# Optimization experiments

Hardware: AMD Instinct MI355X
Metric: run time of the kernel (lower is better)

Reference implementation:

```python
import jax, jax.numpy as jnp
import numpy as np

N = 100000
E = 1600000
IN_C = 512
OUT_C = 128


def setup_inputs() -> dict:
    key = jax.random.key(0)
    k1, k2, k3, k4 = jax.random.split(key, 4)
    x = jax.random.normal(k1, (N, IN_C), dtype=jnp.float32)
    edge_index = jax.random.randint(k2, (2, E), 0, N, dtype=jnp.int64)
    # GCNConv parameters (glorot weight, zero bias as in PyG defaults)
    scale = jnp.sqrt(6.0 / (IN_C + OUT_C)).astype(jnp.float32)
    W = jax.random.uniform(k3, (IN_C, OUT_C), dtype=jnp.float32, minval=-scale, maxval=scale)
    b = jnp.zeros((OUT_C,), dtype=jnp.float32)
    return {"x": x, "edge_index": edge_index, "W": W, "b": b}


def reference(x, edge_index, W, b):
    n = x.shape[0]
    loops = jnp.arange(n, dtype=edge_index.dtype)
    src = jnp.concatenate([edge_index[0], loops])  # [E+N] message sources
    dst = jnp.concatenate([edge_index[1], loops])  # [E+N] message targets
    # symmetric GCN normalization: deg over targets incl. self-loops
    deg = jax.ops.segment_sum(jnp.ones_like(src, dtype=x.dtype), dst, num_segments=n)
    dinv = jnp.where(deg > 0, jax.lax.rsqrt(deg), 0.0)
    norm = dinv[src] * dinv[dst]  # [E+N]
    h = x @ W  # [N, OUT_C] transform first (in > out)
    msg = h[src] * norm[:, None]  # [E+N, OUT_C]
    out = jax.ops.segment_sum(msg, dst, num_segments=n) + b
    return (out, 0)
```

## Files before the change

### kernel.cpp

```cpp
#include <hip/hip_runtime.h>

#define IN_C 512
#define OUT_C 128
#define NB 128
#define CHUNK 8192

typedef float f32x4 __attribute__((ext_vector_type(4)));
typedef __bf16 bf16x8 __attribute__((ext_vector_type(8)));

static inline int cdiv(int a, int b) { return (a + b - 1) / b; }

__device__ __forceinline__ unsigned short bfbits(__bf16 h) {
  return __builtin_bit_cast(unsigned short, h);
}


__global__ __launch_bounds__(256) void hist_kernel(const int* __restrict__ dst,
                                                   int* __restrict__ table,
                                                   int nchunks, int E) {
  __shared__ int hcnt[NB];
  int t = threadIdx.x;
  int c = blockIdx.x;
  if (t < NB) hcnt[t] = 0;
  __syncthreads();
  int base = c * CHUNK;
  for (int i = t; i < CHUNK; i += 256) {
    int e = base + i;
    if (e < E) atomicAdd(&hcnt[dst[e] >> 10], 1);
  }
  __syncthreads();
  if (t < NB) table[t * nchunks + c] = hcnt[t];
}

__global__ __launch_bounds__(256) void tscan_kernel(int* __restrict__ table,
                                                    int* __restrict__ bstart,
                                                    int nchunks, int E) {
  __shared__ int sh[256];
  int t = threadIdx.x;
  int total = NB * nchunks;
  int S = (total + 255) / 256;
  int lo = t * S;
  int hi = lo + S; if (hi > total) hi = total;
  int s = 0;
  int i = lo;
  for (; i + 4 <= hi; i += 4)
    s += table[i] + table[i + 1] + table[i + 2] + table[i + 3];
  for (; i < hi; i++) s += table[i];
  sh[t] = s;
  __syncthreads();
  for (int off = 1; off < 256; off <<= 1) {
    int x = sh[t];
    if (t >= off) x += sh[t - off];
    __syncthreads();
    sh[t] = x;
    __syncthreads();
  }
  int run = sh[t] - s;
  for (i = lo; i < hi; i++) {
    int v = table[i];
    table[i] = run;
    run += v;
  }
  __syncthreads();
  for (int b = t; b < NB; b += 256) bstart[b] = table[b * nchunks];
  if (t == 0) bstart[NB] = E;
}

__global__ __launch_bounds__(256) void scat2_kernel(const int* __restrict__ src,
                                                    const int* __restrict__ dst,
                                                    const int* __restrict__ table,
                                                    int* __restrict__ inter,
                                                    int nchunks, int E) {
  __shared__ int cur[NB];
  int t = threadIdx.x;
  int c = blockIdx.x;
  if (t < NB) cur[t] = table[t * nchunks + c];
  __syncthreads();
  int base = c * CHUNK;
  for (int i = t; i < CHUNK; i += 256) {
    int e = base + i;
    if (e < E) {
      int d = dst[e];
      int pos = atomicAdd(&cur[d >> 10], 1);
      inter[pos] = (src[e] << 10) | (d & 1023);
    }
  }
}

__global__ __launch_bounds__(256) void bdeg_offs_kernel(const int* __restrict__ inter,
                                                        const int* __restrict__ bstart,
                                                        int* __restrict__ offs,
                                                        float* __restrict__ dinv,
                                                        int n, int E, int nbk) {
  __shared__ int dl[1024];
  __shared__ int sh[256];
  int t = threadIdx.x;
  int b = blockIdx.x;
  for (int i = t; i < 1024; i += 256) dl[i] = 0;
  __syncthreads();
  int lo = bstart[b], hi = bstart[b + 1];
  for (int e = lo + t; e < hi; e += 256) atomicAdd(&dl[inter[e] & 1023], 1);
  __syncthreads();
  int c[4];
  int s = 0;
#pragma unroll
  for (int j = 0; j < 4; j++) {
    c[j] = dl[t * 4 + j];
    s += c[j];
  }
  sh[t] = s;
  __syncthreads();
  for (int off = 1; off < 256; off <<= 1) {
    int x = sh[t];
    if (t >= off) x += sh[t - off];
    __syncthreads();
    sh[t] = x;
    __syncthreads();
  }
  int run = sh[t] - s + lo;
  int nb0 = b << 10;
#pragma unroll
  for (int j = 0; j < 4; j++) {
    int node = nb0 + t * 4 + j;
    if (node < n) {
      offs[node] = run;
      dinv[node] = rsqrtf((float)c[j] + 1.0f);
    }
    run += c[j];
  }
  if (b == nbk - 1 && t == 255) offs[n] = E;
}

__global__ __launch_bounds__(256) void scat3_kernel(const int* __restrict__ inter,
                                                    const int* __restrict__ bstart,
                                                    const int* __restrict__ offs,
                                                    int* __restrict__ csr_src, int n) {
  __shared__ int cur[1024];
  int t = threadIdx.x;
  int b = blockIdx.x;
  int nb0 = b << 10;
  for (int i = t; i < 1024; i += 256) {
    int node = nb0 + i;
    cur[i] = (node < n) ? offs[node] : 0;
  }
  __syncthreads();
  int lo = bstart[b], hi = bstart[b + 1];
  for (int e = lo + t; e < hi; e += 256) {
    int u = inter[e];
    int pos = atomicAdd(&cur[u & 1023], 1);
    csr_src[pos] = u >> 10;
  }
}

__global__ __launch_bounds__(256) void wsplit_kernel(const float* __restrict__ W,
                                                     unsigned short* __restrict__ wfh,
                                                     unsigned short* __restrict__ wfl) {
  int i = blockIdx.x * 256 + threadIdx.x;
  if (i >= IN_C * OUT_C) return;
  int k = i >> 7;
  int col = i & 127;
  float w = W[i];
  __bf16 hb = (__bf16)w;
  __bf16 lb = (__bf16)(w - (float)hb);
  int ks = k >> 5;
  int lg = (k & 31) >> 3;
  int j = k & 7;
  int cb = col >> 4;
  int lane = lg * 16 + (col & 15);
  size_t idx = ((size_t)(ks * 8 + cb) * 64 + lane) * 8 + j;
  wfh[idx] = bfbits(hb);
  wfl[idx] = bfbits(lb);
}

__global__ __launch_bounds__(256) void gemm_mfma_kernel(
    const float* __restrict__ x, const unsigned short* __restrict__ wfh,
    const unsigned short* __restrict__ wfl, const float* __restrict__ dinv,
    unsigned short* __restrict__ h, int n) {
  __shared__ float xs[2][4096];

  const int tid = threadIdx.x;
  const int wv = tid >> 6;
  const int lane = tid & 63;
  const int l15 = lane & 15;
  const int lg = lane >> 4;
  const int wr = wv >> 1;
  const int wc = wv & 1;
  const int row0 = blockIdx.x * 128;

  const float* gsrc[4];
#pragma unroll
  for (int i = 0; i < 4; i++) {
    int pslot = i * 256 + tid;
    int row = pslot >> 3;
    int q = pslot & 7;
    int s = q ^ (row & 7);
    int grow = row0 + row;
    if (grow > n - 1) grow = n - 1;
    gsrc[i] = x + (size_t)grow * IN_C + s * 4;
  }

  const unsigned short* bph = wfh + ((size_t)(wc * 4) * 64 + lane) * 8;
  const unsigned short* bpl = wfl + ((size_t)(wc * 4) * 64 + lane) * 8;

  f32x4 acc[4][4];
#pragma unroll
  for (int i = 0; i < 4; i++)
#pragma unroll
    for (int j = 0; j < 4; j++) acc[i][j] = (f32x4)0.0f;

#pragma unroll
  for (int i = 0; i < 4; i++) {
    char* lp = (char*)&xs[0][0] + i * 4096 + wv * 1024;
    __builtin_amdgcn_global_load_lds(
        (const __attribute__((address_space(1))) void*)gsrc[i],
        (__attribute__((address_space(3))) void*)lp, 16, 0, 0);
    gsrc[i] += 32;
  }
  __syncthreads();

  int cur = 0;
  for (int ks = 0; ks < 16; ks++) {
    if (ks < 15) {
#pragma unroll
      for (int i = 0; i < 4; i++) {
        char* lp = (char*)&xs[cur ^ 1][0] + i * 4096 + wv * 1024;
        __builtin_amdgcn_global_load_lds(
            (const __attribute__((address_space(1))) void*)gsrc[i],
            (__attribute__((address_space(3))) void*)lp, 16, 0, 0);
        gsrc[i] += 32;
      }
    }
    bf16x8 bh[4], bl[4];
#pragma unroll
    for (int nt = 0; nt < 4; nt++) {
      bh[nt] = __builtin_bit_cast(bf16x8, *(const uint4*)(bph + (size_t)ks * 4096 + nt * 512));
      bl[nt] = __builtin_bit_cast(bf16x8, *(const uint4*)(bpl + (size_t)ks * 4096 + nt * 512));
    }
    const float* bp = &xs[cur][0];
    bf16x8 ah[4];
#pragma unroll
    for (int rt = 0; rt < 4; rt++) {
      int row = wr * 64 + rt * 16 + l15;
      int r7 = row & 7;
      int s0 = (lg * 2) ^ r7;
      int s1 = (lg * 2 + 1) ^ r7;
      float4 f0 = *(const float4*)(bp + row * 32 + s0 * 4);
      float4 f1 = *(const float4*)(bp + row * 32 + s1 * 4);
      float f[8] = {f0.x, f0.y, f0.z, f0.w, f1.x, f1.y, f1.z, f1.w};
      bf16x8 hh;
#pragma unroll
      for (int j = 0; j < 8; j++) hh[j] = (__bf16)f[j];
      ah[rt] = hh;
    }
#pragma unroll
    for (int rt = 0; rt < 4; rt++)
#pragma unroll
      for (int nt = 0; nt < 4; nt++) {
        acc[rt][nt] = __builtin_amdgcn_mfma_f32_16x16x32_bf16(ah[rt], bh[nt], acc[rt][nt], 0, 0, 0);
        acc[rt][nt] = __builtin_amdgcn_mfma_f32_16x16x32_bf16(ah[rt], bl[nt], acc[rt][nt], 0, 0, 0);
      }
    __syncthreads();
    cur ^= 1;
  }

#pragma unroll
  for (int rt = 0; rt < 4; rt++) {
    int rowbase = row0 + wr * 64 + rt * 16 + lg * 4;
#pragma unroll
    for (int r = 0; r < 4; r++) {
      int row = rowbase + r;
      if (row < n) {
        float di = dinv[row];
#pragma unroll
        for (int nt = 0; nt < 4; nt++) {
          int col = wc * 64 + nt * 16 + l15;
          h[(size_t)row * OUT_C + col] = bfbits((__bf16)(acc[rt][nt][r] * di));
        }
      }
    }
  }
}

__device__ __forceinline__ float bflo(unsigned int u) {
  return __builtin_bit_cast(float, u << 16);
}
__device__ __forceinline__ float bfhi(unsigned int u) {
  return __builtin_bit_cast(float, u & 0xffff0000u);
}

__global__ __launch_bounds__(256) void gather_kernel(const int* __restrict__ offs,
                                                     const int* __restrict__ csr_src,
                                                     const unsigned short* __restrict__ h,
                                                     const float* __restrict__ dinv,
                                                     const float* __restrict__ b,
                                                     float* __restrict__ out,
                                                     int n, int tail) {
  int wid = threadIdx.x >> 6;
  int lane = threadIdx.x & 63;
  int l15 = lane & 15;
  int q = lane >> 4;
  int node = blockIdx.x * 4 + wid;
  if (node >= n) return;

  int start = offs[node];
  int end = offs[node + 1];

  float ax0 = 0, ay0 = 0, ax1 = 0, ay1 = 0, ax2 = 0, ay2 = 0, ax3 = 0, ay3 = 0;

  int e = start + q;
  for (; e + 4 < end; e += 8) {
    int s0 = csr_src[e];
    int s1 = csr_src[e + 4];
    uint4 u0 = *(const uint4*)(h + (size_t)s0 * OUT_C + l15 * 8);
    uint4 u1 = *(const uint4*)(h + (size_t)s1 * OUT_C + l15 * 8);
    ax0 += bflo(u0.x) + bflo(u1.x); ay0 += bfhi(u0.x) + bfhi(u1.x);
    ax1 += bflo(u0.y) + bflo(u1.y); ay1 += bfhi(u0.y) + bfhi(u1.y);
    ax2 += bflo(u0.z) + bflo(u1.z); ay2 += bfhi(u0.z) + bfhi(u1.z);
    ax3 += bflo(u0.w) + bflo(u1.w); ay3 += bfhi(u0.w) + bfhi(u1.w);
  }
  if (e < end) {
    int s0 = csr_src[e];
    uint4 u0 = *(const uint4*)(h + (size_t)s0 * OUT_C + l15 * 8);
    ax0 += bflo(u0.x); ay0 += bfhi(u0.x);
    ax1 += bflo(u0.y); ay1 += bfhi(u0.y);
    ax2 += bflo(u0.z); ay2 += bfhi(u0.z);
    ax3 += bflo(u0.w); ay3 += bfhi(u0.w);
  }

#pragma unroll
  for (int mask = 16; mask <= 32; mask <<= 1) {
    ax0 += __shfl_xor(ax0, mask); ay0 += __shfl_xor(ay0, mask);
    ax1 += __shfl_xor(ax1, mask); ay1 += __shfl_xor(ay1, mask);
    ax2 += __shfl_xor(ax2, mask); ay2 += __shfl_xor(ay2, mask);
    ax3 += __shfl_xor(ax3, mask); ay3 += __shfl_xor(ay3, mask);
  }

  float dd = dinv[node];
  uint4 us = *(const uint4*)(h + (size_t)node * OUT_C + l15 * 8);
  ax0 = (ax0 + bflo(us.x)) * dd; ay0 = (ay0 + bfhi(us.x)) * dd;
  ax1 = (ax1 + bflo(us.y)) * dd; ay1 = (ay1 + bfhi(us.y)) * dd;
  ax2 = (ax2 + bflo(us.z)) * dd; ay2 = (ay2 + bfhi(us.z)) * dd;
  ax3 = (ax3 + bflo(us.w)) * dd; ay3 = (ay3 + bfhi(us.w)) * dd;

  if (q == 0) {
    float4 b0 = *(const float4*)(b + l15 * 8);
    float4 b1 = *(const float4*)(b + l15 * 8 + 4);
    float4 o0 = make_float4(ax0 + b0.x, ay0 + b0.y, ax1 + b0.z, ay1 + b0.w);
    float4 o1 = make_float4(ax2 + b1.x, ay2 + b1.y, ax3 + b1.z, ay3 + b1.w);
    float* op = out + (size_t)node * OUT_C + l15 * 8;
    *(float4*)op = o0;
    *(float4*)(op + 4) = o1;
  }

  if (node == 0 && lane == 0) {
    for (int t = 0; t < tail; t++) out[(size_t)n * OUT_C + t] = 0.0f;
  }
}

extern "C" void kernel_launch(void* const* d_in, const int* in_sizes, int n_in,
                              void* d_out, int out_size, void* d_ws, size_t ws_size,
                              hipStream_t stream) {
  const float* x = (const float*)d_in[0];
  const int* ei = (const int*)d_in[1];
  const float* W = (const float*)d_in[2];
  const float* b = (const float*)d_in[3];

  const int n = in_sizes[0] / IN_C;
  const int E = in_sizes[1] / 2;
  const int* src = ei;
  const int* dst = ei + E;
  float* out = (float*)d_out;

  const int nchunks = cdiv(E, CHUNK);
  const int nbk = cdiv(n, 1024);

  size_t p = 0;
  auto alloc = [&](size_t bytes) { size_t o = p; p += (bytes + 255) & ~(size_t)255; return o; };
  char* ws = (char*)d_ws;
  float*          dinv   = (float*)(ws + alloc((size_t)n * 4));
  int*            offs   = (int*)(ws + alloc(((size_t)n + 1) * 4));
  int*            csrsrc = (int*)(ws + alloc((size_t)E * 4));
  int*            bstart = (int*)(ws + alloc((NB + 1) * 4));
  unsigned short* wfh    = (unsigned short*)(ws + alloc((size_t)IN_C * OUT_C * 2));
  unsigned short* wfl    = (unsigned short*)(ws + alloc((size_t)IN_C * OUT_C * 2));
  size_t upos = p;
  int*            inter  = (int*)(ws + upos);
  int*            table  = (int*)(ws + upos + (((size_t)E * 4 + 255) & ~(size_t)255));
  unsigned short* h      = (unsigned short*)(ws + upos);

  wsplit_kernel<<<cdiv(IN_C * OUT_C, 256), 256, 0, stream>>>(W, wfh, wfl);
  hist_kernel<<<nchunks, 256, 0, stream>>>(dst, table, nchunks, E);
  tscan_kernel<<<1, 256, 0, stream>>>(table, bstart, nchunks, E);
  scat2_kernel<<<nchunks, 256, 0, stream>>>(src, dst, table, inter, nchunks, E);
  bdeg_offs_kernel<<<nbk, 256, 0, stream>>>(inter, bstart, offs, dinv, n, E, nbk);
  scat3_kernel<<<nbk, 256, 0, stream>>>(inter, bstart, offs, csrsrc, n);
  gemm_mfma_kernel<<<cdiv(n, 128), 256, 0, stream>>>(x, wfh, wfl, dinv, h, n);
  int tail = out_size - n * OUT_C;
  gather_kernel<<<cdiv(n, 4), 256, 0, stream>>>(offs, csrsrc, h, dinv, b, out, n, tail);
}
```

Baseline: 268.4 us.

## Refine GEMM pipeline waits, unroll gather by four, enlarge histogram chunk

The GEMM main loop replaces the two __syncthreads per step with raw s_barrier and explicit vmcnt waits. The weight fragment loads are also issued before the next LDS prefetch, so global-to-LDS copies and B loads overlap better. The CSR aggregation kernel now gathers four neighbor rows per iteration instead of two, for more memory-level parallelism, and the tail becomes a loop. CHUNK doubles, changing how many edge chunks the histogram/partition kernels use. Hand-coded vmcnt counts risk correctness if the compiler reorders or changes the load counts.

```diff
diff --git a/kernel.cpp b/kernel.cpp
--- a/kernel.cpp
+++ b/kernel.cpp
@@ -3,7 +3,7 @@
 #define IN_C 512
 #define OUT_C 128
 #define NB 128
-#define CHUNK 8192
+#define CHUNK 16384
 
 typedef float f32x4 __attribute__((ext_vector_type(4)));
 typedef __bf16 bf16x8 __attribute__((ext_vector_type(8)));
@@ -216,27 +216,31 @@
         (__attribute__((address_space(3))) void*)lp, 16, 0, 0);
     gsrc[i] += 32;
   }
-  __syncthreads();
-
-  int cur = 0;
+
   for (int ks = 0; ks < 16; ks++) {
+    __builtin_amdgcn_s_barrier();
+    bf16x8 bh[4], bl[4];
+#pragma unroll
+    for (int nt = 0; nt < 4; nt++) {
+      bh[nt] = __builtin_bit_cast(bf16x8, *(const uint4*)(bph + (size_t)ks * 4096 + nt * 512));
+      bl[nt] = __builtin_bit_cast(bf16x8, *(const uint4*)(bpl + (size_t)ks * 4096 + nt * 512));
+    }
     if (ks < 15) {
 #pragma unroll
       for (int i = 0; i < 4; i++) {
-        char* lp = (char*)&xs[cur ^ 1][0] + i * 4096 + wv * 1024;
+        char* lp = (char*)&xs[(ks + 1) & 1][0] + i * 4096 + wv * 1024;
         __builtin_amdgcn_global_load_lds(
             (const __attribute__((address_space(1))) void*)gsrc[i],
             (__attribute__((address_space(3))) void*)lp, 16, 0, 0);
         gsrc[i] += 32;
       }
-    }
-    bf16x8 bh[4], bl[4];
-#pragma unroll
-    for (int nt = 0; nt < 4; nt++) {
-      bh[nt] = __builtin_bit_cast(bf16x8, *(const uint4*)(bph + (size_t)ks * 4096 + nt * 512));
-      bl[nt] = __builtin_bit_cast(bf16x8, *(const uint4*)(bpl + (size_t)ks * 4096 + nt * 512));
-    }
-    const float* bp = &xs[cur][0];
+      asm volatile("s_waitcnt vmcnt(12)" ::: "memory");
+    } else {
+      asm volatile("s_waitcnt vmcnt(8)" ::: "memory");
+    }
+    __builtin_amdgcn_s_barrier();
+
+    const float* bp = &xs[ks & 1][0];
     bf16x8 ah[4];
 #pragma unroll
     for (int rt = 0; rt < 4; rt++) {
@@ -259,8 +263,6 @@
         acc[rt][nt] = __builtin_amdgcn_mfma_f32_16x16x32_bf16(ah[rt], bh[nt], acc[rt][nt], 0, 0, 0);
         acc[rt][nt] = __builtin_amdgcn_mfma_f32_16x16x32_bf16(ah[rt], bl[nt], acc[rt][nt], 0, 0, 0);
       }
-    __syncthreads();
-    cur ^= 1;
   }
 
 #pragma unroll
@@ -308,17 +310,25 @@
   float ax0 = 0, ay0 = 0, ax1 = 0, ay1 = 0, ax2 = 0, ay2 = 0, ax3 = 0, ay3 = 0;
 
   int e = start + q;
-  for (; e + 4 < end; e += 8) {
+  for (; e + 12 < end; e += 16) {
     int s0 = csr_src[e];
     int s1 = csr_src[e + 4];
+    int s2 = csr_src[e + 8];
+    int s3 = csr_src[e + 12];
     uint4 u0 = *(const uint4*)(h + (size_t)s0 * OUT_C + l15 * 8);
     uint4 u1 = *(const uint4*)(h + (size_t)s1 * OUT_C + l15 * 8);
-    ax0 += bflo(u0.x) + bflo(u1.x); ay0 += bfhi(u0.x) + bfhi(u1.x);
-    ax1 += bflo(u0.y) + bflo(u1.y); ay1 += bfhi(u0.y) + bfhi(u1.y);
-    ax2 += bflo(u0.z) + bflo(u1.z); ay2 += bfhi(u0.z) + bfhi(u1.z);
-    ax3 += bflo(u0.w) + bflo(u1.w); ay3 += bfhi(u0.w) + bfhi(u1.w);
-  }
-  if (e < end) {
+    uint4 u2 = *(const uint4*)(h + (size_t)s2 * OUT_C + l15 * 8);
+    uint4 u3 = *(const uint4*)(h + (size_t)s3 * OUT_C + l15 * 8);
+    ax0 += (bflo(u0.x) + bflo(u1.x)) + (bflo(u2.x) + bflo(u3.x));
+    ay0 += (bfhi(u0.x) + bfhi(u1.x)) + (bfhi(u2.x) + bfhi(u3.x));
+    ax1 += (bflo(u0.y) + bflo(u1.y)) + (bflo(u2.y) + bflo(u3.y));
+    ay1 += (bfhi(u0.y) + bfhi(u1.y)) + (bfhi(u2.y) + bfhi(u3.y));
+    ax2 += (bflo(u0.z) + bflo(u1.z)) + (bflo(u2.z) + bflo(u3.z));
+    ay2 += (bfhi(u0.z) + bfhi(u1.z)) + (bfhi(u2.z) + bfhi(u3.z));
+    ax3 += (bflo(u0.w) + bflo(u1.w)) + (bflo(u2.w) + bflo(u3.w));
+    ay3 += (bfhi(u0.w) + bfhi(u1.w)) + (bfhi(u2.w) + bfhi(u3.w));
+  }
+  for (; e < end; e += 4) {
     int s0 = csr_src[e];
     uint4 u0 = *(const uint4*)(h + (size_t)s0 * OUT_C + l15 * 8);
     ax0 += bflo(u0.x); ay0 += bfhi(u0.x);
```

New measurement: 281.3 us. 4.8% more time.
